# Performance work log

Measured on AMD Instinct MI355X. Metric: run time of the kernel, lower is better.

## Reference

```python
import jax, jax.numpy as jnp
import numpy as np

N, M, P, H = 200000, 20, 64, 256
EPS = 1e-12  # inside sqrt: avoids NaN grads when duplicate neighbors give zero distance


def setup_inputs() -> dict:
    key = jax.random.key(0)
    ks = jax.random.split(key, 8)
    x = jax.random.normal(ks[0], (N, P), jnp.float32)
    pos = jax.random.uniform(ks[1], (N, 2), jnp.float32) * 10.0
    y = jax.random.normal(ks[2], (N,), jnp.float32)
    # m distinct-from-self neighbor indices per node (offset trick avoids self loops)
    off = jax.random.randint(ks[3], (N, M), 1, N)
    nbr_idx = ((jnp.arange(N)[:, None] + off) % N).astype(jnp.int32)
    theta = jnp.array([1.0, 1.0, 0.1], jnp.float32)  # (sigma_sq, phi, tau)
    w1 = jax.random.normal(ks[4], (P, H), jnp.float32) * (1.0 / np.sqrt(P))
    b1 = jnp.zeros((H,), jnp.float32)
    w2 = jax.random.normal(ks[5], (H, 1), jnp.float32) * (1.0 / np.sqrt(H))
    b2 = jnp.zeros((1,), jnp.float32)
    return dict(x=x, pos=pos, y=y, nbr_idx=nbr_idx, theta=theta,
                w1=w1, b1=b1, w2=w2, b2=b2)


def _dist(a, b):
    return jnp.sqrt(jnp.sum((a - b) ** 2, axis=-1) + EPS)


def reference(x, pos, y, nbr_idx, theta, w1, b1, w2, b2):
    sigma_sq, phi, tau = theta[0], theta[1], theta[2]
    tau_sq = tau * sigma_sq
    m = nbr_idx.shape[1]
    pos_nbr = pos[nbr_idx]                                            # [N,M,2] gather
    # Cov(i, N(i)): exponential covariance of node-to-neighbor distances  [N,M]
    cov_i_ni = sigma_sq * jnp.exp(-phi * _dist(pos[:, None, :], pos_nbr))
    # Cov(N(i), N(i)) + nugget on the diagonal                          [N,M,M]
    d_nn = _dist(pos_nbr[:, :, None, :], pos_nbr[:, None, :, :])
    cov = sigma_sq * jnp.exp(-phi * d_nn) + tau_sq * jnp.eye(m, dtype=pos.dtype)
    # B_i = Cov(N,N)^{-1} Cov(i,N)  (batched small solve == inv @ vec)  [N,M]
    b_i = jnp.linalg.solve(cov, cov_i_ni[..., None])[..., 0]
    f_i = sigma_sq + tau - jnp.sum(b_i * cov_i_ni, axis=1)             # [N]
    inv_sqrt_f = 1.0 / jnp.sqrt(f_i)
    # MLP: Linear -> ReLU -> Linear, squeezed to [N]
    o = (jax.nn.relu(x @ w1 + b1) @ w2 + b2)[:, 0]
    y_decor = (y - jnp.sum(y[nbr_idx] * b_i, axis=1)) * inv_sqrt_f
    o_decor = (o - jnp.sum(o[nbr_idx] * b_i, axis=1)) * inv_sqrt_f
    return (y_decor, o_decor, o)
```

## Files before the change

kernel.cpp:

```cpp
#include <hip/hip_runtime.h>


#define MM   20
#define PP   64
#define HH   256
#define EPSF 1e-12f

#define CSE(j, r) csx[2*(j)*((j)+1) + (r)]
#define C20(r)    csx[60 + (r)]

typedef __attribute__((ext_vector_type(8))) short bf16x8;
typedef __attribute__((ext_vector_type(4))) float f32x4;

static __device__ __forceinline__ unsigned short f2bf(float f) {
    unsigned int u = __builtin_bit_cast(unsigned int, f);
    u += 0x7fffu + ((u >> 16) & 1u);
    return (unsigned short)(u >> 16);
}
static __device__ __forceinline__ float bf2f(unsigned short h) {
    unsigned int u = ((unsigned int)h) << 16;
    return __builtin_bit_cast(float, u);
}

__global__ __launch_bounds__(256, 2)
void mlp_mfma_kernel(const float* __restrict__ x,
                     const float* __restrict__ w1,
                     const float* __restrict__ b1,
                     const float* __restrict__ w2,
                     const float* __restrict__ b2,
                     float* __restrict__ o_out, int n)
{
    __shared__ __align__(16) short swh[PP * HH];
    __shared__ __align__(16) short swl[PP * HH];
    __shared__ float sb1[HH];
    __shared__ float sw2[HH];
    const int tid = threadIdx.x;

    {
        const int col = tid;
        const int t = col >> 4, nn = col & 15;
        #pragma unroll
        for (int g = 0; g < 8; ++g) {
            const int s = g >> 2, q = g & 3;
            bf16x8 hv, lv;
            #pragma unroll
            for (int u = 0; u < 8; ++u) {
                float v = w1[(g * 8 + u) * HH + col];
                unsigned short h = f2bf(v);
                hv[u] = (short)h;
                lv[u] = (short)f2bf(v - bf2f(h));
            }
            const int base = ((((t * 2 + s) * 4 + q) * 16) + nn) * 8;
            *(bf16x8*)&swh[base] = hv;
            *(bf16x8*)&swl[base] = lv;
        }
        sb1[tid] = b1[tid];
        sw2[tid] = w2[tid];
    }
    __syncthreads();

    const int lane = tid & 63;
    const int wv   = tid >> 6;
    const int nn   = lane & 15;
    const int q    = lane >> 4;
    const int wb   = blockIdx.x * 128 + wv * 32;

    bf16x8 ah[2][2], al[2][2];
    #pragma unroll
    for (int mt = 0; mt < 2; ++mt) {
        const int row = wb + mt * 16 + nn;
        #pragma unroll
        for (int s = 0; s < 2; ++s) {
            float v[8];
            if (row < n) {
                const float* xp = x + (size_t)row * PP + s * 32 + q * 8;
                float4 va = *(const float4*)(xp);
                float4 vb = *(const float4*)(xp + 4);
                v[0]=va.x; v[1]=va.y; v[2]=va.z; v[3]=va.w;
                v[4]=vb.x; v[5]=vb.y; v[6]=vb.z; v[7]=vb.w;
            } else {
                #pragma unroll
                for (int u = 0; u < 8; ++u) v[u] = 0.0f;
            }
            bf16x8 h, l;
            #pragma unroll
            for (int u = 0; u < 8; ++u) {
                unsigned short hb = f2bf(v[u]);
                h[u] = (short)hb;
                l[u] = (short)f2bf(v[u] - bf2f(hb));
            }
            ah[mt][s] = h;
            al[mt][s] = l;
        }
    }

    float part[2][4];
    #pragma unroll
    for (int mt = 0; mt < 2; ++mt)
        #pragma unroll
        for (int r = 0; r < 4; ++r) part[mt][r] = 0.0f;

    #pragma unroll
    for (int t = 0; t < 16; ++t) {
        f32x4 acc[2];
        #pragma unroll
        for (int mt = 0; mt < 2; ++mt) acc[mt] = (f32x4)(0.0f);
        #pragma unroll
        for (int s = 0; s < 2; ++s) {
            const int fb = ((((t * 2 + s) * 4 + q) * 16) + nn) * 8;
            bf16x8 bh = *(const bf16x8*)&swh[fb];
            bf16x8 bl = *(const bf16x8*)&swl[fb];
            #pragma unroll
            for (int mt = 0; mt < 2; ++mt) {
                acc[mt] = __builtin_amdgcn_mfma_f32_16x16x32_bf16(ah[mt][s], bh, acc[mt], 0, 0, 0);
                acc[mt] = __builtin_amdgcn_mfma_f32_16x16x32_bf16(al[mt][s], bh, acc[mt], 0, 0, 0);
                acc[mt] = __builtin_amdgcn_mfma_f32_16x16x32_bf16(ah[mt][s], bl, acc[mt], 0, 0, 0);
            }
        }
        const float b1t = sb1[t * 16 + nn];
        const float w2t = sw2[t * 16 + nn];
        #pragma unroll
        for (int mt = 0; mt < 2; ++mt)
            #pragma unroll
            for (int r = 0; r < 4; ++r)
                part[mt][r] = fmaf(fmaxf(acc[mt][r] + b1t, 0.0f), w2t, part[mt][r]);
    }

    #pragma unroll
    for (int w = 1; w < 16; w <<= 1)
        #pragma unroll
        for (int mt = 0; mt < 2; ++mt)
            #pragma unroll
            for (int r = 0; r < 4; ++r)
                part[mt][r] += __shfl_xor(part[mt][r], w, 64);

    const float bb = b2[0];
    if (nn == 0) {
        #pragma unroll
        for (int mt = 0; mt < 2; ++mt) {
            const int row = wb + mt * 16 + q * 4;
            if (row < n) {
                float4 o4 = make_float4(part[mt][0] + bb, part[mt][1] + bb,
                                        part[mt][2] + bb, part[mt][3] + bb);
                *(float4*)&o_out[row] = o4;
            }
        }
    }
}

#define QSWZ(v, s) __builtin_bit_cast(float, __builtin_amdgcn_ds_swizzle( \
    __builtin_bit_cast(int, (v)), 0x8000 | (0x55 * (s))))

#define GATH(R) mall[R] = QSWZ(mv[(R) >> 2], (R) & 3);

#define SCASE(K, P) case K: {                                              \
    _Pragma("unroll")                                                      \
    for (int j = (P); j < 5; ++j) pk[j] = CSE(j, (K));                     \
    p20 = C20(K); pbv = bv[K];                                             \
    pd  = QSWZ(pk[(P)], (K) & 3);                                          \
} break;

__global__ __launch_bounds__(256, 2)
void solve_kernel(const float* __restrict__ pos,
                  const float* __restrict__ y,
                  const int*   __restrict__ nbr,
                  const float* __restrict__ theta,
                  const float* __restrict__ o_in,
                  float* __restrict__ yd,
                  float* __restrict__ od, int n)
{
    const int tid  = threadIdx.x;
    const int h_   = tid & 3;
    const int i    = blockIdx.x * 64 + (tid >> 2);
    if (i >= n) return;

    const float sigma_sq = theta[0];
    const float phi      = theta[1];
    const float tau      = theta[2];
    const float tau_sq   = tau * sigma_sq;

    const float L2E = 1.44269504088896340736f;
    const float c1  = -phi * L2E;
    const float c0  = __builtin_amdgcn_logf(sigma_sq);

    const float sqrtEPS = __builtin_amdgcn_sqrtf(EPSF);
    const float diagA   = __builtin_amdgcn_exp2f(fmaf(sqrtEPS, c1, c0)) + tau_sq;
    const float diagB   = sigma_sq + tau;

    int idx[MM];
    const int4* nb4 = (const int4*)(nbr + (size_t)i * MM);
    #pragma unroll
    for (int k = 0; k < MM / 4; ++k) {
        int4 v = nb4[k];
        idx[4*k] = v.x; idx[4*k+1] = v.y; idx[4*k+2] = v.z; idx[4*k+3] = v.w;
    }

    float px[21], py[21];
    const float2* pos2 = (const float2*)pos;
    #pragma unroll
    for (int j = 0; j < MM; ++j) {
        float2 p = pos2[idx[j]];
        px[j] = p.x; py[j] = p.y;
    }
    {
        float2 p = pos2[i];
        px[20] = p.x; py[20] = p.y;
    }

    float cx[5], cy[5];
    #pragma unroll
    for (int j = 0; j < 5; ++j) {
        int cj = nbr[(size_t)i * MM + 4*j + h_];
        float2 p = pos2[cj];
        cx[j] = p.x; cy[j] = p.y;
    }

    float bv[21];
    {
        const float* src = (h_ & 1) ? o_in : y;
        #pragma unroll
        for (int j = 0; j < MM; ++j) bv[j] = src[idx[j]];
        bv[20] = src[i];
    }

    float csx[81];
    #pragma unroll
    for (int j = 0; j < 5; ++j) {
        #pragma unroll
        for (int r = 0; r <= 4*j + 3; ++r) {
            float dx = px[r] - cx[j];
            float dy = py[r] - cy[j];
            float d  = __builtin_amdgcn_sqrtf(fmaf(dx, dx, fmaf(dy, dy, EPSF)));
            float v  = __builtin_amdgcn_exp2f(fmaf(d, c1, c0));
            v = (r == 4*j + h_) ? diagA : v;
            CSE(j, r) = v;
        }
    }
    #pragma unroll
    for (int r = 0; r < 20; ++r) {
        float dx = px[r] - px[20];
        float dy = py[r] - py[20];
        float d  = __builtin_amdgcn_sqrtf(fmaf(dx, dx, fmaf(dy, dy, EPSF)));
        C20(r)   = __builtin_amdgcn_exp2f(fmaf(d, c1, c0));
    }
    C20(20) = diagB;

    float pk[5], mv[5], mall[21], p20, pbv, pd;

    #pragma unroll 1
    for (int k = 0; k < 4; ++k) {
        switch (k) {
        SCASE(0,0) SCASE(1,0) SCASE(2,0) SCASE(3,0)
        default: break;
        }
        float rp = __builtin_amdgcn_rcpf(pd);
        rp = rp * (2.0f - pd * rp);
        #pragma unroll
        for (int j = 0; j < 5; ++j)
            mv[j] = (4*j + h_ > k) ? pk[j] * rp : 0.0f;
        GATH(0)  GATH(1)  GATH(2)  GATH(3)  GATH(4)  GATH(5)  GATH(6)
        GATH(7)  GATH(8)  GATH(9)  GATH(10) GATH(11) GATH(12) GATH(13)
        GATH(14) GATH(15) GATH(16) GATH(17) GATH(18) GATH(19)
        mall[20] = p20 * rp;
        #pragma unroll
        for (int j = 0; j < 5; ++j) {
            float pkj = pk[j];
            #pragma unroll
            for (int r = 0; r <= 4*j + 3; ++r)
                CSE(j, r) = fmaf(-mall[r], pkj, CSE(j, r));
        }
        #pragma unroll
        for (int r = 0; r <= 20; ++r) {
            C20(r) = fmaf(-mall[r], p20, C20(r));
            bv[r]  = fmaf(-mall[r], pbv, bv[r]);
        }
    }

    #pragma unroll 1
    for (int k = 4; k < 8; ++k) {
        switch (k) {
        SCASE(4,1) SCASE(5,1) SCASE(6,1) SCASE(7,1)
        default: break;
        }
        float rp = __builtin_amdgcn_rcpf(pd);
        rp = rp * (2.0f - pd * rp);
        #pragma unroll
        for (int j = 1; j < 5; ++j)
            mv[j] = (4*j + h_ > k) ? pk[j] * rp : 0.0f;
        GATH(4)  GATH(5)  GATH(6)  GATH(7)  GATH(8)  GATH(9)  GATH(10)
        GATH(11) GATH(12) GATH(13) GATH(14) GATH(15) GATH(16) GATH(17)
        GATH(18) GATH(19)
        mall[20] = p20 * rp;
        #pragma unroll
        for (int j = 1; j < 5; ++j) {
            float pkj = pk[j];
            #pragma unroll
            for (int r = 4; r <= 4*j + 3; ++r)
                CSE(j, r) = fmaf(-mall[r], pkj, CSE(j, r));
        }
        #pragma unroll
        for (int r = 4; r <= 20; ++r) {
            C20(r) = fmaf(-mall[r], p20, C20(r));
            bv[r]  = fmaf(-mall[r], pbv, bv[r]);
        }
    }

    #pragma unroll 1
    for (int k = 8; k < 12; ++k) {
        switch (k) {
        SCASE(8,2) SCASE(9,2) SCASE(10,2) SCASE(11,2)
        default: break;
        }
        float rp = __builtin_amdgcn_rcpf(pd);
        rp = rp * (2.0f - pd * rp);
        #pragma unroll
        for (int j = 2; j < 5; ++j)
            mv[j] = (4*j + h_ > k) ? pk[j] * rp : 0.0f;
        GATH(8)  GATH(9)  GATH(10) GATH(11) GATH(12) GATH(13) GATH(14)
        GATH(15) GATH(16) GATH(17) GATH(18) GATH(19)
        mall[20] = p20 * rp;
        #pragma unroll
        for (int j = 2; j < 5; ++j) {
            float pkj = pk[j];
            #pragma unroll
            for (int r = 8; r <= 4*j + 3; ++r)
                CSE(j, r) = fmaf(-mall[r], pkj, CSE(j, r));
        }
        #pragma unroll
        for (int r = 8; r <= 20; ++r) {
            C20(r) = fmaf(-mall[r], p20, C20(r));
            bv[r]  = fmaf(-mall[r], pbv, bv[r]);
        }
    }

    #pragma unroll 1
    for (int k = 12; k < 16; ++k) {
        switch (k) {
        SCASE(12,3) SCASE(13,3) SCASE(14,3) SCASE(15,3)
        default: break;
        }
        float rp = __builtin_amdgcn_rcpf(pd);
        rp = rp * (2.0f - pd * rp);
        #pragma unroll
        for (int j = 3; j < 5; ++j)
            mv[j] = (4*j + h_ > k) ? pk[j] * rp : 0.0f;
        GATH(12) GATH(13) GATH(14) GATH(15) GATH(16) GATH(17) GATH(18)
        GATH(19)
        mall[20] = p20 * rp;
        #pragma unroll
        for (int j = 3; j < 5; ++j) {
            float pkj = pk[j];
            #pragma unroll
            for (int r = 12; r <= 4*j + 3; ++r)
                CSE(j, r) = fmaf(-mall[r], pkj, CSE(j, r));
        }
        #pragma unroll
        for (int r = 12; r <= 20; ++r) {
            C20(r) = fmaf(-mall[r], p20, C20(r));
            bv[r]  = fmaf(-mall[r], pbv, bv[r]);
        }
    }

    #pragma unroll 1
    for (int k = 16; k < 20; ++k) {
        switch (k) {
        SCASE(16,4) SCASE(17,4) SCASE(18,4) SCASE(19,4)
        default: break;
        }
        float rp = __builtin_amdgcn_rcpf(pd);
        rp = rp * (2.0f - pd * rp);
        mv[4] = (16 + h_ > k) ? pk[4] * rp : 0.0f;
        GATH(16) GATH(17) GATH(18) GATH(19)
        mall[20] = p20 * rp;
        {
            float pkj = pk[4];
            #pragma unroll
            for (int r = 16; r <= 19; ++r)
                CSE(4, r) = fmaf(-mall[r], pkj, CSE(4, r));
        }
        #pragma unroll
        for (int r = 16; r <= 20; ++r) {
            C20(r) = fmaf(-mall[r], p20, C20(r));
            bv[r]  = fmaf(-mall[r], pbv, bv[r]);
        }
    }

    float f  = C20(20);
    float is = __builtin_amdgcn_rsqf(f);
    is = is * fmaf(-0.5f * f * is, is, 1.5f);

    if (h_ == 0)      yd[i] = bv[20] * is;
    else if (h_ == 1) od[i] = bv[20] * is;
}

extern "C" void kernel_launch(void* const* d_in, const int* in_sizes, int n_in,
                              void* d_out, int out_size, void* d_ws, size_t ws_size,
                              hipStream_t stream)
{
    const float* x     = (const float*)d_in[0];
    const float* pos   = (const float*)d_in[1];
    const float* y     = (const float*)d_in[2];
    const int*   nbr   = (const int*)  d_in[3];
    const float* theta = (const float*)d_in[4];
    const float* w1    = (const float*)d_in[5];
    const float* b1    = (const float*)d_in[6];
    const float* w2    = (const float*)d_in[7];
    const float* b2    = (const float*)d_in[8];

    const int n = in_sizes[2];
    float* out = (float*)d_out;
    float* yd = out;
    float* od = out + (size_t)n;
    float* oo = out + 2 * (size_t)n;

    mlp_mfma_kernel<<<(n + 127) / 128, 256, 0, stream>>>(x, w1, b1, w2, b2, oo, n);
    solve_kernel<<<(n + 63) / 64, 256, 0, stream>>>(pos, y, nbr, theta, oo, yd, od, n);
}
```

Baseline: 195.8 us.

## Split the augmented column and RHS across lane pairs to raise solver occupancy

The solve kernel previously kept the full 21-entry augmented column (C20) and the RHS vector (bv) replicated in each of the 4 lanes per node. Each lane pair now holds half of these rows (11 each), and the pivot, RHS and gather values are fetched with ds_swizzle patterns. This cuts VGPR use by about 40 registers per lane, which allows raising launch bounds from 2 to 3 blocks per SIMD. In exchange it adds extra swizzles and re-reads neighbor indices and positions to build the split arrays.

```diff
diff --git a/kernel.cpp b/kernel.cpp
--- a/kernel.cpp
+++ b/kernel.cpp
@@ -7,7 +7,6 @@
 #define EPSF 1e-12f
 
 #define CSE(j, r) csx[2*(j)*((j)+1) + (r)]
-#define C20(r)    csx[60 + (r)]
 
 typedef __attribute__((ext_vector_type(8))) short bf16x8;
 typedef __attribute__((ext_vector_type(4))) float f32x4;
@@ -148,19 +147,23 @@
     }
 }
 
-#define QSWZ(v, s) __builtin_bit_cast(float, __builtin_amdgcn_ds_swizzle( \
-    __builtin_bit_cast(int, (v)), 0x8000 | (0x55 * (s))))
-
-#define GATH(R) mall[R] = QSWZ(mv[(R) >> 2], (R) & 3);
+#define QSWZ(v, pat) __builtin_bit_cast(float, __builtin_amdgcn_ds_swizzle( \
+    __builtin_bit_cast(int, (v)), 0x8000 | (pat)))
+
+#define GATH(R) mall[R] = QSWZ(mv[(R) >> 2], 0x55 * ((R) & 3));
+#define BMG(S)  bm[S]   = QSWZ(mv[(S) >> 1], ((S) & 1) ? 0xFA : 0x50);
 
 #define SCASE(K, P) case K: {                                              \
     _Pragma("unroll")                                                      \
     for (int j = (P); j < 5; ++j) pk[j] = CSE(j, (K));                     \
-    p20 = C20(K); pbv = bv[K];                                             \
-    pd  = QSWZ(pk[(P)], (K) & 3);                                          \
+    float pbs = bvl[(K) >> 1];                                             \
+    float p2s = c20l[(K) >> 1];                                            \
+    pd  = QSWZ(pk[(P)], 0x55 * ((K) & 3));                                 \
+    pbv = QSWZ(pbs, ((K) & 1) ? 0xEE : 0x44);                              \
+    p20 = QSWZ(p2s, ((K) & 1) ? 0xAA : 0x00);                              \
 } break;
 
-__global__ __launch_bounds__(256, 2)
+__global__ __launch_bounds__(256, 3)
 void solve_kernel(const float* __restrict__ pos,
                   const float* __restrict__ y,
                   const int*   __restrict__ nbr,
@@ -171,6 +174,7 @@
 {
     const int tid  = threadIdx.x;
     const int h_   = tid & 3;
+    const int q2   = h_ >> 1;
     const int i    = blockIdx.x * 64 + (tid >> 2);
     if (i >= n) return;
 
@@ -215,15 +219,24 @@
         cx[j] = p.x; cy[j] = p.y;
     }
 
-    float bv[21];
+    float bvl[11], c20l[11];
     {
         const float* src = (h_ & 1) ? o_in : y;
         #pragma unroll
-        for (int j = 0; j < MM; ++j) bv[j] = src[idx[j]];
-        bv[20] = src[i];
-    }
-
-    float csx[81];
+        for (int s = 0; s < 10; ++s) {
+            int jr = nbr[(size_t)i * MM + 2*s + q2];
+            bvl[s] = src[jr];
+            float2 p = pos2[jr];
+            float dx = p.x - px[20];
+            float dy = p.y - py[20];
+            float d  = __builtin_amdgcn_sqrtf(fmaf(dx, dx, fmaf(dy, dy, EPSF)));
+            c20l[s]  = __builtin_amdgcn_exp2f(fmaf(d, c1, c0));
+        }
+        bvl[10]  = q2 ? 0.0f : src[i];
+        c20l[10] = q2 ? 0.0f : diagB;
+    }
+
+    float csx[60];
     #pragma unroll
     for (int j = 0; j < 5; ++j) {
         #pragma unroll
@@ -236,16 +249,8 @@
             CSE(j, r) = v;
         }
     }
-    #pragma unroll
-    for (int r = 0; r < 20; ++r) {
-        float dx = px[r] - px[20];
-        float dy = py[r] - py[20];
-        float d  = __builtin_amdgcn_sqrtf(fmaf(dx, dx, fmaf(dy, dy, EPSF)));
-        C20(r)   = __builtin_amdgcn_exp2f(fmaf(d, c1, c0));
-    }
-    C20(20) = diagB;
-
-    float pk[5], mv[5], mall[21], p20, pbv, pd;
+
+    float pk[5], mv[5], mall[20], bm[11], p20, pbv, pd;
 
     #pragma unroll 1
     for (int k = 0; k < 4; ++k) {
@@ -261,7 +266,8 @@
         GATH(0)  GATH(1)  GATH(2)  GATH(3)  GATH(4)  GATH(5)  GATH(6)
         GATH(7)  GATH(8)  GATH(9)  GATH(10) GATH(11) GATH(12) GATH(13)
         GATH(14) GATH(15) GATH(16) GATH(17) GATH(18) GATH(19)
-        mall[20] = p20 * rp;
+        BMG(0) BMG(1) BMG(2) BMG(3) BMG(4) BMG(5) BMG(6) BMG(7) BMG(8) BMG(9)
+        bm[10] = p20 * rp;
         #pragma unroll
         for (int j = 0; j < 5; ++j) {
             float pkj = pk[j];
@@ -270,9 +276,9 @@
                 CSE(j, r) = fmaf(-mall[r], pkj, CSE(j, r));
         }
         #pragma unroll
-        for (int r = 0; r <= 20; ++r) {
-            C20(r) = fmaf(-mall[r], p20, C20(r));
-            bv[r]  = fmaf(-mall[r], pbv, bv[r]);
+        for (int s = 0; s <= 10; ++s) {
+            c20l[s] = fmaf(-bm[s], p20, c20l[s]);
+            bvl[s]  = fmaf(-bm[s], pbv, bvl[s]);
         }
     }
 
@@ -290,7 +296,8 @@
         GATH(4)  GATH(5)  GATH(6)  GATH(7)  GATH(8)  GATH(9)  GATH(10)
         GATH(11) GATH(12) GATH(13) GATH(14) GATH(15) GATH(16) GATH(17)
         GATH(18) GATH(19)
-        mall[20] = p20 * rp;
+        BMG(2) BMG(3) BMG(4) BMG(5) BMG(6) BMG(7) BMG(8) BMG(9)
+        bm[10] = p20 * rp;
         #pragma unroll
         for (int j = 1; j < 5; ++j) {
             float pkj = pk[j];
@@ -299,9 +306,9 @@
                 CSE(j, r) = fmaf(-mall[r], pkj, CSE(j, r));
         }
         #pragma unroll
-        for (int r = 4; r <= 20; ++r) {
-            C20(r) = fmaf(-mall[r], p20, C20(r));
-            bv[r]  = fmaf(-mall[r], pbv, bv[r]);
+        for (int s = 2; s <= 10; ++s) {
+            c20l[s] = fmaf(-bm[s], p20, c20l[s]);
+            bvl[s]  = fmaf(-bm[s], pbv, bvl[s]);
         }
     }
 
@@ -318,7 +325,8 @@
             mv[j] = (4*j + h_ > k) ? pk[j] * rp : 0.0f;
         GATH(8)  GATH(9)  GATH(10) GATH(11) GATH(12) GATH(13) GATH(14)
         GATH(15) GATH(16) GATH(17) GATH(18) GATH(19)
-        mall[20] = p20 * rp;
+        BMG(4) BMG(5) BMG(6) BMG(7) BMG(8) BMG(9)
+        bm[10] = p20 * rp;
         #pragma unroll
         for (int j = 2; j < 5; ++j) {
             float pkj = pk[j];
@@ -327,9 +335,9 @@
                 CSE(j, r) = fmaf(-mall[r], pkj, CSE(j, r));
         }
         #pragma unroll
-        for (int r = 8; r <= 20; ++r) {
-            C20(r) = fmaf(-mall[r], p20, C20(r));
-            bv[r]  = fmaf(-mall[r], pbv, bv[r]);
+        for (int s = 4; s <= 10; ++s) {
+            c20l[s] = fmaf(-bm[s], p20, c20l[s]);
+            bvl[s]  = fmaf(-bm[s], pbv, bvl[s]);
         }
     }
 
@@ -346,7 +354,8 @@
             mv[j] = (4*j + h_ > k) ? pk[j] * rp : 0.0f;
         GATH(12) GATH(13) GATH(14) GATH(15) GATH(16) GATH(17) GATH(18)
         GATH(19)
-        mall[20] = p20 * rp;
+        BMG(6) BMG(7) BMG(8) BMG(9)
+        bm[10] = p20 * rp;
         #pragma unroll
         for (int j = 3; j < 5; ++j) {
             float pkj = pk[j];
@@ -355,9 +364,9 @@
                 CSE(j, r) = fmaf(-mall[r], pkj, CSE(j, r));
         }
         #pragma unroll
-        for (int r = 12; r <= 20; ++r) {
-            C20(r) = fmaf(-mall[r], p20, C20(r));
-            bv[r]  = fmaf(-mall[r], pbv, bv[r]);
+        for (int s = 6; s <= 10; ++s) {
+            c20l[s] = fmaf(-bm[s], p20, c20l[s]);
+            bvl[s]  = fmaf(-bm[s], pbv, bvl[s]);
         }
     }
 
@@ -371,7 +380,8 @@
         rp = rp * (2.0f - pd * rp);
         mv[4] = (16 + h_ > k) ? pk[4] * rp : 0.0f;
         GATH(16) GATH(17) GATH(18) GATH(19)
-        mall[20] = p20 * rp;
+        BMG(8) BMG(9)
+        bm[10] = p20 * rp;
         {
             float pkj = pk[4];
             #pragma unroll
@@ -379,18 +389,18 @@
                 CSE(4, r) = fmaf(-mall[r], pkj, CSE(4, r));
         }
         #pragma unroll
-        for (int r = 16; r <= 20; ++r) {
-            C20(r) = fmaf(-mall[r], p20, C20(r));
-            bv[r]  = fmaf(-mall[r], pbv, bv[r]);
-        }
-    }
-
-    float f  = C20(20);
+        for (int s = 8; s <= 10; ++s) {
+            c20l[s] = fmaf(-bm[s], p20, c20l[s]);
+            bvl[s]  = fmaf(-bm[s], pbv, bvl[s]);
+        }
+    }
+
+    float f  = c20l[10];
     float is = __builtin_amdgcn_rsqf(f);
     is = is * fmaf(-0.5f * f * is, is, 1.5f);
 
-    if (h_ == 0)      yd[i] = bv[20] * is;
-    else if (h_ == 1) od[i] = bv[20] * is;
+    if (h_ == 0)      yd[i] = bvl[10] * is;
+    else if (h_ == 1) od[i] = bvl[10] * is;
 }
 
 extern "C" void kernel_launch(void* const* d_in, const int* in_sizes, int n_in,
```

Result: slower. 219.2 us (+12.0%).

## Co-schedule MLP and covariance solve in one launch; apply weights in epilogue

Applied to the files above, without the earlier changes.

Merges the MLP and solve kernels into one launch whose blocks are interleaved (one MLP block per two solve blocks), so MFMA work and VALU-heavy factorization can overlap on the GPU. The solve no longer carries y/o right-hand sides through elimination. Instead it back-substitutes for b_i, scales by 1/sqrt(f) and writes weights to workspace. A new epilogue kernel gathers y and o at the neighbors and applies those weights. This removes the dependency of the solve on the MLP output. The cost is an extra workspace write and read of about 24 floats per node, plus a serial back-substitution with shuffles.

```diff
diff --git a/kernel.cpp b/kernel.cpp
--- a/kernel.cpp
+++ b/kernel.cpp
@@ -5,6 +5,7 @@
 #define PP   64
 #define HH   256
 #define EPSF 1e-12f
+#define WSTR 24
 
 #define CSE(j, r) csx[2*(j)*((j)+1) + (r)]
 #define C20(r)    csx[60 + (r)]
@@ -22,170 +23,411 @@
     return __builtin_bit_cast(float, u);
 }
 
+#define QSWZ(v, pat) __builtin_bit_cast(float, __builtin_amdgcn_ds_swizzle( \
+    __builtin_bit_cast(int, (v)), 0x8000 | (pat)))
+
+#define GATH(R) mall[R] = QSWZ(mv[(R) >> 2], 0x55 * ((R) & 3));
+
+#define SCASE(K, P) case K: {                                              \
+    _Pragma("unroll")                                                      \
+    for (int j = (P); j < 5; ++j) pk[j] = CSE(j, (K));                     \
+    p20 = C20(K);                                                          \
+    pd  = QSWZ(pk[(P)], 0x55 * ((K) & 3));                                 \
+} break;
+
+#define BSTEP(R, JMIN) {                                                   \
+    float acc = 0.0f;                                                      \
+    _Pragma("unroll")                                                      \
+    for (int j = (JMIN); j < 5; ++j) {                                     \
+        float t = CSE(j, (R)) * bl[j];                                     \
+        acc += (4*j + h_ > (R)) ? t : 0.0f;                                \
+    }                                                                      \
+    acc += __shfl_xor(acc, 1, 64);                                         \
+    acc += __shfl_xor(acc, 2, 64);                                         \
+    float pdr = QSWZ(CSE((R) >> 2, (R)), 0x55 * ((R) & 3));                \
+    float rr = __builtin_amdgcn_rcpf(pdr);                                 \
+    rr = rr * (2.0f - pdr * rr);                                           \
+    float bR = (C20(R) - acc) * rr;                                        \
+    if (((R) & 3) == h_) bl[(R) >> 2] = bR;                                \
+}
+
 __global__ __launch_bounds__(256, 2)
-void mlp_mfma_kernel(const float* __restrict__ x,
-                     const float* __restrict__ w1,
-                     const float* __restrict__ b1,
-                     const float* __restrict__ w2,
-                     const float* __restrict__ b2,
-                     float* __restrict__ o_out, int n)
+void fused_kernel(const float* __restrict__ x,
+                  const float* __restrict__ w1,
+                  const float* __restrict__ b1,
+                  const float* __restrict__ w2,
+                  const float* __restrict__ b2,
+                  const float* __restrict__ pos,
+                  const int*   __restrict__ nbr,
+                  const float* __restrict__ theta,
+                  float* __restrict__ o_out,
+                  float* __restrict__ wis,
+                  int n, int nm)
 {
     __shared__ __align__(16) short swh[PP * HH];
     __shared__ __align__(16) short swl[PP * HH];
     __shared__ float sb1[HH];
     __shared__ float sw2[HH];
+
+    const int b   = blockIdx.x;
+    const int grp = b / 3;
+    const int rem = b - grp * 3;
     const int tid = threadIdx.x;
 
+    if (rem == 1 && grp < nm) {
+        {
+            const int col = tid;
+            const int t = col >> 4, nn = col & 15;
+            #pragma unroll
+            for (int g = 0; g < 8; ++g) {
+                const int s = g >> 2, q = g & 3;
+                bf16x8 hv, lv;
+                #pragma unroll
+                for (int u = 0; u < 8; ++u) {
+                    float v = w1[(g * 8 + u) * HH + col];
+                    unsigned short h = f2bf(v);
+                    hv[u] = (short)h;
+                    lv[u] = (short)f2bf(v - bf2f(h));
+                }
+                const int base = ((((t * 2 + s) * 4 + q) * 16) + nn) * 8;
+                *(bf16x8*)&swh[base] = hv;
+                *(bf16x8*)&swl[base] = lv;
+            }
+            sb1[tid] = b1[tid];
+            sw2[tid] = w2[tid];
+        }
+        __syncthreads();
+
+        const int lane = tid & 63;
+        const int wv   = tid >> 6;
+        const int nn   = lane & 15;
+        const int q    = lane >> 4;
+        const int wb   = grp * 128 + wv * 32;
+
+        bf16x8 ah[2][2], al[2][2];
+        #pragma unroll
+        for (int mt = 0; mt < 2; ++mt) {
+            const int row = wb + mt * 16 + nn;
+            #pragma unroll
+            for (int s = 0; s < 2; ++s) {
+                float v[8];
+                if (row < n) {
+                    const float* xp = x + (size_t)row * PP + s * 32 + q * 8;
+                    float4 va = *(const float4*)(xp);
+                    float4 vb = *(const float4*)(xp + 4);
+                    v[0]=va.x; v[1]=va.y; v[2]=va.z; v[3]=va.w;
+                    v[4]=vb.x; v[5]=vb.y; v[6]=vb.z; v[7]=vb.w;
+                } else {
+                    #pragma unroll
+                    for (int u = 0; u < 8; ++u) v[u] = 0.0f;
+                }
+                bf16x8 h, l;
+                #pragma unroll
+                for (int u = 0; u < 8; ++u) {
+                    unsigned short hb = f2bf(v[u]);
+                    h[u] = (short)hb;
+                    l[u] = (short)f2bf(v[u] - bf2f(hb));
+                }
+                ah[mt][s] = h;
+                al[mt][s] = l;
+            }
+        }
+
+        float part[2][4];
+        #pragma unroll
+        for (int mt = 0; mt < 2; ++mt)
+            #pragma unroll
+            for (int r = 0; r < 4; ++r) part[mt][r] = 0.0f;
+
+        #pragma unroll
+        for (int t = 0; t < 16; ++t) {
+            f32x4 acc[2];
+            #pragma unroll
+            for (int mt = 0; mt < 2; ++mt) acc[mt] = (f32x4)(0.0f);
+            #pragma unroll
+            for (int s = 0; s < 2; ++s) {
+                const int fb = ((((t * 2 + s) * 4 + q) * 16) + nn) * 8;
+                bf16x8 bh = *(const bf16x8*)&swh[fb];
+                bf16x8 bl2 = *(const bf16x8*)&swl[fb];
+                #pragma unroll
+                for (int mt = 0; mt < 2; ++mt) {
+                    acc[mt] = __builtin_amdgcn_mfma_f32_16x16x32_bf16(ah[mt][s], bh,  acc[mt], 0, 0, 0);
+                    acc[mt] = __builtin_amdgcn_mfma_f32_16x16x32_bf16(al[mt][s], bh,  acc[mt], 0, 0, 0);
+                    acc[mt] = __builtin_amdgcn_mfma_f32_16x16x32_bf16(ah[mt][s], bl2, acc[mt], 0, 0, 0);
+                }
+            }
+            const float b1t = sb1[t * 16 + nn];
+            const float w2t = sw2[t * 16 + nn];
+            #pragma unroll
+            for (int mt = 0; mt < 2; ++mt)
+                #pragma unroll
+                for (int r = 0; r < 4; ++r)
+                    part[mt][r] = fmaf(fmaxf(acc[mt][r] + b1t, 0.0f), w2t, part[mt][r]);
+        }
+
+        #pragma unroll
+        for (int w = 1; w < 16; w <<= 1)
+            #pragma unroll
+            for (int mt = 0; mt < 2; ++mt)
+                #pragma unroll
+                for (int r = 0; r < 4; ++r)
+                    part[mt][r] += __shfl_xor(part[mt][r], w, 64);
+
+        const float bb = b2[0];
+        if (nn == 0) {
+            #pragma unroll
+            for (int mt = 0; mt < 2; ++mt) {
+                const int row = wb + mt * 16 + q * 4;
+                if (row < n) {
+                    float4 o4 = make_float4(part[mt][0] + bb, part[mt][1] + bb,
+                                            part[mt][2] + bb, part[mt][3] + bb);
+                    *(float4*)&o_out[row] = o4;
+                }
+            }
+        }
+        return;
+    }
+
     {
-        const int col = tid;
-        const int t = col >> 4, nn = col & 15;
-        #pragma unroll
-        for (int g = 0; g < 8; ++g) {
-            const int s = g >> 2, q = g & 3;
-            bf16x8 hv, lv;
-            #pragma unroll
-            for (int u = 0; u < 8; ++u) {
-                float v = w1[(g * 8 + u) * HH + col];
-                unsigned short h = f2bf(v);
-                hv[u] = (short)h;
-                lv[u] = (short)f2bf(v - bf2f(h));
-            }
-            const int base = ((((t * 2 + s) * 4 + q) * 16) + nn) * 8;
-            *(bf16x8*)&swh[base] = hv;
-            *(bf16x8*)&swl[base] = lv;
-        }
-        sb1[tid] = b1[tid];
-        sw2[tid] = w2[tid];
+        int mcnt = (b + 1) / 3; if (mcnt > nm) mcnt = nm;
+        const int sidx = b - mcnt;
+        const int h_   = tid & 3;
+        const int i    = sidx * 64 + (tid >> 2);
+        if (i >= n) return;
+
+        const float sigma_sq = theta[0];
+        const float phi      = theta[1];
+        const float tau      = theta[2];
+        const float tau_sq   = tau * sigma_sq;
+
+        const float L2E = 1.44269504088896340736f;
+        const float c1  = -phi * L2E;
+        const float c0  = __builtin_amdgcn_logf(sigma_sq);
+
+        const float sqrtEPS = __builtin_amdgcn_sqrtf(EPSF);
+        const float diagA   = __builtin_amdgcn_exp2f(fmaf(sqrtEPS, c1, c0)) + tau_sq;
+        const float diagB   = sigma_sq + tau;
+
+        int idx[MM];
+        const int4* nb4 = (const int4*)(nbr + (size_t)i * MM);
+        #pragma unroll
+        for (int k = 0; k < MM / 4; ++k) {
+            int4 v = nb4[k];
+            idx[4*k] = v.x; idx[4*k+1] = v.y; idx[4*k+2] = v.z; idx[4*k+3] = v.w;
+        }
+
+        float px[21], py[21];
+        const float2* pos2 = (const float2*)pos;
+        #pragma unroll
+        for (int j = 0; j < MM; ++j) {
+            float2 p = pos2[idx[j]];
+            px[j] = p.x; py[j] = p.y;
+        }
+        {
+            float2 p = pos2[i];
+            px[20] = p.x; py[20] = p.y;
+        }
+
+        float cx[5], cy[5];
+        #pragma unroll
+        for (int j = 0; j < 5; ++j) {
+            int cj = nbr[(size_t)i * MM + 4*j + h_];
+            float2 p = pos2[cj];
+            cx[j] = p.x; cy[j] = p.y;
+        }
+
+        float csx[81];
+        #pragma unroll
+        for (int j = 0; j < 5; ++j) {
+            #pragma unroll
+            for (int r = 0; r <= 4*j + 3; ++r) {
+                float dx = px[r] - cx[j];
+                float dy = py[r] - cy[j];
+                float d  = __builtin_amdgcn_sqrtf(fmaf(dx, dx, fmaf(dy, dy, EPSF)));
+                float v  = __builtin_amdgcn_exp2f(fmaf(d, c1, c0));
+                v = (r == 4*j + h_) ? diagA : v;
+                CSE(j, r) = v;
+            }
+        }
+        #pragma unroll
+        for (int r = 0; r < 20; ++r) {
+            float dx = px[r] - px[20];
+            float dy = py[r] - py[20];
+            float d  = __builtin_amdgcn_sqrtf(fmaf(dx, dx, fmaf(dy, dy, EPSF)));
+            C20(r)   = __builtin_amdgcn_exp2f(fmaf(d, c1, c0));
+        }
+        C20(20) = diagB;
+
+        float pk[5], mv[5], mall[21], p20, pd;
+
+        #pragma unroll 1
+        for (int k = 0; k < 4; ++k) {
+            switch (k) {
+            SCASE(0,0) SCASE(1,0) SCASE(2,0) SCASE(3,0)
+            default: break;
+            }
+            float rp = __builtin_amdgcn_rcpf(pd);
+            rp = rp * (2.0f - pd * rp);
+            #pragma unroll
+            for (int j = 0; j < 5; ++j)
+                mv[j] = (4*j + h_ > k) ? pk[j] * rp : 0.0f;
+            GATH(0)  GATH(1)  GATH(2)  GATH(3)  GATH(4)  GATH(5)  GATH(6)
+            GATH(7)  GATH(8)  GATH(9)  GATH(10) GATH(11) GATH(12) GATH(13)
+            GATH(14) GATH(15) GATH(16) GATH(17) GATH(18) GATH(19)
+            mall[20] = p20 * rp;
+            #pragma unroll
+            for (int j = 0; j < 5; ++j) {
+                float pkj = pk[j];
+                #pragma unroll
+                for (int r = 0; r <= 4*j + 3; ++r)
+                    CSE(j, r) = fmaf(-mall[r], pkj, CSE(j, r));
+            }
+            #pragma unroll
+            for (int r = 0; r <= 20; ++r)
+                C20(r) = fmaf(-mall[r], p20, C20(r));
+        }
+
+        #pragma unroll 1
+        for (int k = 4; k < 8; ++k) {
+            switch (k) {
+            SCASE(4,1) SCASE(5,1) SCASE(6,1) SCASE(7,1)
+            default: break;
+            }
+            float rp = __builtin_amdgcn_rcpf(pd);
+            rp = rp * (2.0f - pd * rp);
+            #pragma unroll
+            for (int j = 1; j < 5; ++j)
+                mv[j] = (4*j + h_ > k) ? pk[j] * rp : 0.0f;
+            GATH(4)  GATH(5)  GATH(6)  GATH(7)  GATH(8)  GATH(9)  GATH(10)
+            GATH(11) GATH(12) GATH(13) GATH(14) GATH(15) GATH(16) GATH(17)
+            GATH(18) GATH(19)
+            mall[20] = p20 * rp;
+            #pragma unroll
+            for (int j = 1; j < 5; ++j) {
+                float pkj = pk[j];
+                #pragma unroll
+                for (int r = 4; r <= 4*j + 3; ++r)
+                    CSE(j, r) = fmaf(-mall[r], pkj, CSE(j, r));
+            }
+            #pragma unroll
+            for (int r = 4; r <= 20; ++r)
+                C20(r) = fmaf(-mall[r], p20, C20(r));
+        }
+
+        #pragma unroll 1
+        for (int k = 8; k < 12; ++k) {
+            switch (k) {
+            SCASE(8,2) SCASE(9,2) SCASE(10,2) SCASE(11,2)
+            default: break;
+            }
+            float rp = __builtin_amdgcn_rcpf(pd);
+            rp = rp * (2.0f - pd * rp);
+            #pragma unroll
+            for (int j = 2; j < 5; ++j)
+                mv[j] = (4*j + h_ > k) ? pk[j] * rp : 0.0f;
+            GATH(8)  GATH(9)  GATH(10) GATH(11) GATH(12) GATH(13) GATH(14)
+            GATH(15) GATH(16) GATH(17) GATH(18) GATH(19)
+            mall[20] = p20 * rp;
+            #pragma unroll
+            for (int j = 2; j < 5; ++j) {
+                float pkj = pk[j];
+                #pragma unroll
+                for (int r = 8; r <= 4*j + 3; ++r)
+                    CSE(j, r) = fmaf(-mall[r], pkj, CSE(j, r));
+            }
+            #pragma unroll
+            for (int r = 8; r <= 20; ++r)
+                C20(r) = fmaf(-mall[r], p20, C20(r));
+        }
+
+        #pragma unroll 1
+        for (int k = 12; k < 16; ++k) {
+            switch (k) {
+            SCASE(12,3) SCASE(13,3) SCASE(14,3) SCASE(15,3)
+            default: break;
+            }
+            float rp = __builtin_amdgcn_rcpf(pd);
+            rp = rp * (2.0f - pd * rp);
+            #pragma unroll
+            for (int j = 3; j < 5; ++j)
+                mv[j] = (4*j + h_ > k) ? pk[j] * rp : 0.0f;
+            GATH(12) GATH(13) GATH(14) GATH(15) GATH(16) GATH(17) GATH(18)
+            GATH(19)
+            mall[20] = p20 * rp;
+            #pragma unroll
+            for (int j = 3; j < 5; ++j) {
+                float pkj = pk[j];
+                #pragma unroll
+                for (int r = 12; r <= 4*j + 3; ++r)
+                    CSE(j, r) = fmaf(-mall[r], pkj, CSE(j, r));
+            }
+            #pragma unroll
+            for (int r = 12; r <= 20; ++r)
+                C20(r) = fmaf(-mall[r], p20, C20(r));
+        }
+
+        #pragma unroll 1
+        for (int k = 16; k < 20; ++k) {
+            switch (k) {
+            SCASE(16,4) SCASE(17,4) SCASE(18,4) SCASE(19,4)
+            default: break;
+            }
+            float rp = __builtin_amdgcn_rcpf(pd);
+            rp = rp * (2.0f - pd * rp);
+            mv[4] = (16 + h_ > k) ? pk[4] * rp : 0.0f;
+            GATH(16) GATH(17) GATH(18) GATH(19)
+            mall[20] = p20 * rp;
+            {
+                float pkj = pk[4];
+                #pragma unroll
+                for (int r = 16; r <= 19; ++r)
+                    CSE(4, r) = fmaf(-mall[r], pkj, CSE(4, r));
+            }
+            #pragma unroll
+            for (int r = 16; r <= 20; ++r)
+                C20(r) = fmaf(-mall[r], p20, C20(r));
+        }
+
+        float bl[5];
+        BSTEP(19,5) BSTEP(18,4) BSTEP(17,4) BSTEP(16,4)
+        BSTEP(15,4) BSTEP(14,3) BSTEP(13,3) BSTEP(12,3)
+        BSTEP(11,3) BSTEP(10,2) BSTEP(9,2)  BSTEP(8,2)
+        BSTEP(7,2)  BSTEP(6,1)  BSTEP(5,1)  BSTEP(4,1)
+        BSTEP(3,1)  BSTEP(2,0)  BSTEP(1,0)  BSTEP(0,0)
+
+        float f  = C20(20);
+        float is = __builtin_amdgcn_rsqf(f);
+        is = is * fmaf(-0.5f * f * is, is, 1.5f);
+
+        float* wp = wis + (size_t)i * WSTR;
+        #pragma unroll
+        for (int j = 0; j < 5; ++j)
+            wp[4*j + h_] = bl[j] * is;
+        if (h_ == 0) wp[20] = is;
     }
-    __syncthreads();
-
-    const int lane = tid & 63;
-    const int wv   = tid >> 6;
-    const int nn   = lane & 15;
-    const int q    = lane >> 4;
-    const int wb   = blockIdx.x * 128 + wv * 32;
-
-    bf16x8 ah[2][2], al[2][2];
-    #pragma unroll
-    for (int mt = 0; mt < 2; ++mt) {
-        const int row = wb + mt * 16 + nn;
-        #pragma unroll
-        for (int s = 0; s < 2; ++s) {
-            float v[8];
-            if (row < n) {
-                const float* xp = x + (size_t)row * PP + s * 32 + q * 8;
-                float4 va = *(const float4*)(xp);
-                float4 vb = *(const float4*)(xp + 4);
-                v[0]=va.x; v[1]=va.y; v[2]=va.z; v[3]=va.w;
-                v[4]=vb.x; v[5]=vb.y; v[6]=vb.z; v[7]=vb.w;
-            } else {
-                #pragma unroll
-                for (int u = 0; u < 8; ++u) v[u] = 0.0f;
-            }
-            bf16x8 h, l;
-            #pragma unroll
-            for (int u = 0; u < 8; ++u) {
-                unsigned short hb = f2bf(v[u]);
-                h[u] = (short)hb;
-                l[u] = (short)f2bf(v[u] - bf2f(hb));
-            }
-            ah[mt][s] = h;
-            al[mt][s] = l;
-        }
+}
+
+__global__ __launch_bounds__(256, 4)
+void epilogue_kernel(const int*   __restrict__ nbr,
+                     const float* __restrict__ y,
+                     const float* __restrict__ o_in,
+                     const float* __restrict__ wis,
+                     float* __restrict__ yd,
+                     float* __restrict__ od, int n)
+{
+    const int i = blockIdx.x * 256 + threadIdx.x;
+    if (i >= n) return;
+
+    float wv_[20];
+    {
+        const float4* w4 = (const float4*)(wis + (size_t)i * WSTR);
+        *(float4*)&wv_[0]  = w4[0];
+        *(float4*)&wv_[4]  = w4[1];
+        *(float4*)&wv_[8]  = w4[2];
+        *(float4*)&wv_[12] = w4[3];
+        *(float4*)&wv_[16] = w4[4];
     }
-
-    float part[2][4];
-    #pragma unroll
-    for (int mt = 0; mt < 2; ++mt)
-        #pragma unroll
-        for (int r = 0; r < 4; ++r) part[mt][r] = 0.0f;
-
-    #pragma unroll
-    for (int t = 0; t < 16; ++t) {
-        f32x4 acc[2];
-        #pragma unroll
-        for (int mt = 0; mt < 2; ++mt) acc[mt] = (f32x4)(0.0f);
-        #pragma unroll
-        for (int s = 0; s < 2; ++s) {
-            const int fb = ((((t * 2 + s) * 4 + q) * 16) + nn) * 8;
-            bf16x8 bh = *(const bf16x8*)&swh[fb];
-            bf16x8 bl = *(const bf16x8*)&swl[fb];
-            #pragma unroll
-            for (int mt = 0; mt < 2; ++mt) {
-                acc[mt] = __builtin_amdgcn_mfma_f32_16x16x32_bf16(ah[mt][s], bh, acc[mt], 0, 0, 0);
-                acc[mt] = __builtin_amdgcn_mfma_f32_16x16x32_bf16(al[mt][s], bh, acc[mt], 0, 0, 0);
-                acc[mt] = __builtin_amdgcn_mfma_f32_16x16x32_bf16(ah[mt][s], bl, acc[mt], 0, 0, 0);
-            }
-        }
-        const float b1t = sb1[t * 16 + nn];
-        const float w2t = sw2[t * 16 + nn];
-        #pragma unroll
-        for (int mt = 0; mt < 2; ++mt)
-            #pragma unroll
-            for (int r = 0; r < 4; ++r)
-                part[mt][r] = fmaf(fmaxf(acc[mt][r] + b1t, 0.0f), w2t, part[mt][r]);
-    }
-
-    #pragma unroll
-    for (int w = 1; w < 16; w <<= 1)
-        #pragma unroll
-        for (int mt = 0; mt < 2; ++mt)
-            #pragma unroll
-            for (int r = 0; r < 4; ++r)
-                part[mt][r] += __shfl_xor(part[mt][r], w, 64);
-
-    const float bb = b2[0];
-    if (nn == 0) {
-        #pragma unroll
-        for (int mt = 0; mt < 2; ++mt) {
-            const int row = wb + mt * 16 + q * 4;
-            if (row < n) {
-                float4 o4 = make_float4(part[mt][0] + bb, part[mt][1] + bb,
-                                        part[mt][2] + bb, part[mt][3] + bb);
-                *(float4*)&o_out[row] = o4;
-            }
-        }
-    }
-}
-
-#define QSWZ(v, s) __builtin_bit_cast(float, __builtin_amdgcn_ds_swizzle( \
-    __builtin_bit_cast(int, (v)), 0x8000 | (0x55 * (s))))
-
-#define GATH(R) mall[R] = QSWZ(mv[(R) >> 2], (R) & 3);
-
-#define SCASE(K, P) case K: {                                              \
-    _Pragma("unroll")                                                      \
-    for (int j = (P); j < 5; ++j) pk[j] = CSE(j, (K));                     \
-    p20 = C20(K); pbv = bv[K];                                             \
-    pd  = QSWZ(pk[(P)], (K) & 3);                                          \
-} break;
-
-__global__ __launch_bounds__(256, 2)
-void solve_kernel(const float* __restrict__ pos,
-                  const float* __restrict__ y,
-                  const int*   __restrict__ nbr,
-                  const float* __restrict__ theta,
-                  const float* __restrict__ o_in,
-                  float* __restrict__ yd,
-                  float* __restrict__ od, int n)
-{
-    const int tid  = threadIdx.x;
-    const int h_   = tid & 3;
-    const int i    = blockIdx.x * 64 + (tid >> 2);
-    if (i >= n) return;
-
-    const float sigma_sq = theta[0];
-    const float phi      = theta[1];
-    const float tau      = theta[2];
-    const float tau_sq   = tau * sigma_sq;
-
-    const float L2E = 1.44269504088896340736f;
-    const float c1  = -phi * L2E;
-    const float c0  = __builtin_amdgcn_logf(sigma_sq);
-
-    const float sqrtEPS = __builtin_amdgcn_sqrtf(EPSF);
-    const float diagA   = __builtin_amdgcn_exp2f(fmaf(sqrtEPS, c1, c0)) + tau_sq;
-    const float diagB   = sigma_sq + tau;
+    const float is = wis[(size_t)i * WSTR + 20];
 
     int idx[MM];
     const int4* nb4 = (const int4*)(nbr + (size_t)i * MM);
@@ -195,202 +437,14 @@
         idx[4*k] = v.x; idx[4*k+1] = v.y; idx[4*k+2] = v.z; idx[4*k+3] = v.w;
     }
 
-    float px[21], py[21];
-    const float2* pos2 = (const float2*)pos;
+    float sy = 0.0f, so = 0.0f;
     #pragma unroll
     for (int j = 0; j < MM; ++j) {
-        float2 p = pos2[idx[j]];
-        px[j] = p.x; py[j] = p.y;
+        sy = fmaf(wv_[j], y[idx[j]],    sy);
+        so = fmaf(wv_[j], o_in[idx[j]], so);
     }
-    {
-        float2 p = pos2[i];
-        px[20] = p.x; py[20] = p.y;
-    }
-
-    float cx[5], cy[5];
-    #pragma unroll
-    for (int j = 0; j < 5; ++j) {
-        int cj = nbr[(size_t)i * MM + 4*j + h_];
-        float2 p = pos2[cj];
-        cx[j] = p.x; cy[j] = p.y;
-    }
-
-    float bv[21];
-    {
-        const float* src = (h_ & 1) ? o_in : y;
-        #pragma unroll
-        for (int j = 0; j < MM; ++j) bv[j] = src[idx[j]];
-        bv[20] = src[i];
-    }
-
-    float csx[81];
-    #pragma unroll
-    for (int j = 0; j < 5; ++j) {
-        #pragma unroll
-        for (int r = 0; r <= 4*j + 3; ++r) {
-            float dx = px[r] - cx[j];
-            float dy = py[r] - cy[j];
-            float d  = __builtin_amdgcn_sqrtf(fmaf(dx, dx, fmaf(dy, dy, EPSF)));
-            float v  = __builtin_amdgcn_exp2f(fmaf(d, c1, c0));
-            v = (r == 4*j + h_) ? diagA : v;
-            CSE(j, r) = v;
-        }
-    }
-    #pragma unroll
-    for (int r = 0; r < 20; ++r) {
-        float dx = px[r] - px[20];
-        float dy = py[r] - py[20];
-        float d  = __builtin_amdgcn_sqrtf(fmaf(dx, dx, fmaf(dy, dy, EPSF)));
-        C20(r)   = __builtin_amdgcn_exp2f(fmaf(d, c1, c0));
-    }
-    C20(20) = diagB;
-
-    float pk[5], mv[5], mall[21], p20, pbv, pd;
-
-    #pragma unroll 1
-    for (int k = 0; k < 4; ++k) {
-        switch (k) {
-        SCASE(0,0) SCASE(1,0) SCASE(2,0) SCASE(3,0)
-        default: break;
-        }
-        float rp = __builtin_amdgcn_rcpf(pd);
-        rp = rp * (2.0f - pd * rp);
-        #pragma unroll
-        for (int j = 0; j < 5; ++j)
-            mv[j] = (4*j + h_ > k) ? pk[j] * rp : 0.0f;
-        GATH(0)  GATH(1)  GATH(2)  GATH(3)  GATH(4)  GATH(5)  GATH(6)
-        GATH(7)  GATH(8)  GATH(9)  GATH(10) GATH(11) GATH(12) GATH(13)
-        GATH(14) GATH(15) GATH(16) GATH(17) GATH(18) GATH(19)
-        mall[20] = p20 * rp;
-        #pragma unroll
-        for (int j = 0; j < 5; ++j) {
-            float pkj = pk[j];
-            #pragma unroll
-            for (int r = 0; r <= 4*j + 3; ++r)
-                CSE(j, r) = fmaf(-mall[r], pkj, CSE(j, r));
-        }
-        #pragma unroll
-        for (int r = 0; r <= 20; ++r) {
-            C20(r) = fmaf(-mall[r], p20, C20(r));
-            bv[r]  = fmaf(-mall[r], pbv, bv[r]);
-        }
-    }
-
-    #pragma unroll 1
-    for (int k = 4; k < 8; ++k) {
-        switch (k) {
-        SCASE(4,1) SCASE(5,1) SCASE(6,1) SCASE(7,1)
-        default: break;
-        }
-        float rp = __builtin_amdgcn_rcpf(pd);
-        rp = rp * (2.0f - pd * rp);
-        #pragma unroll
-        for (int j = 1; j < 5; ++j)
-            mv[j] = (4*j + h_ > k) ? pk[j] * rp : 0.0f;
-        GATH(4)  GATH(5)  GATH(6)  GATH(7)  GATH(8)  GATH(9)  GATH(10)
-        GATH(11) GATH(12) GATH(13) GATH(14) GATH(15) GATH(16) GATH(17)
-        GATH(18) GATH(19)
-        mall[20] = p20 * rp;
-        #pragma unroll
-        for (int j = 1; j < 5; ++j) {
-            float pkj = pk[j];
-            #pragma unroll
-            for (int r = 4; r <= 4*j + 3; ++r)
-                CSE(j, r) = fmaf(-mall[r], pkj, CSE(j, r));
-        }
-        #pragma unroll
-        for (int r = 4; r <= 20; ++r) {
-            C20(r) = fmaf(-mall[r], p20, C20(r));
-            bv[r]  = fmaf(-mall[r], pbv, bv[r]);
-        }
-    }
-
-    #pragma unroll 1
-    for (int k = 8; k < 12; ++k) {
-        switch (k) {
-        SCASE(8,2) SCASE(9,2) SCASE(10,2) SCASE(11,2)
-        default: break;
-        }
-        float rp = __builtin_amdgcn_rcpf(pd);
-        rp = rp * (2.0f - pd * rp);
-        #pragma unroll
-        for (int j = 2; j < 5; ++j)
-            mv[j] = (4*j + h_ > k) ? pk[j] * rp : 0.0f;
-        GATH(8)  GATH(9)  GATH(10) GATH(11) GATH(12) GATH(13) GATH(14)
-        GATH(15) GATH(16) GATH(17) GATH(18) GATH(19)
-        mall[20] = p20 * rp;
-        #pragma unroll
-        for (int j = 2; j < 5; ++j) {
-            float pkj = pk[j];
-            #pragma unroll
-            for (int r = 8; r <= 4*j + 3; ++r)
-                CSE(j, r) = fmaf(-mall[r], pkj, CSE(j, r));
-        }
-        #pragma unroll
-        for (int r = 8; r <= 20; ++r) {
-            C20(r) = fmaf(-mall[r], p20, C20(r));
-            bv[r]  = fmaf(-mall[r], pbv, bv[r]);
-        }
-    }
-
-    #pragma unroll 1
-    for (int k = 12; k < 16; ++k) {
-        switch (k) {
-        SCASE(12,3) SCASE(13,3) SCASE(14,3) SCASE(15,3)
-        default: break;
-        }
-        float rp = __builtin_amdgcn_rcpf(pd);
-        rp = rp * (2.0f - pd * rp);
-        #pragma unroll
-        for (int j = 3; j < 5; ++j)
-            mv[j] = (4*j + h_ > k) ? pk[j] * rp : 0.0f;
-        GATH(12) GATH(13) GATH(14) GATH(15) GATH(16) GATH(17) GATH(18)
-        GATH(19)
-        mall[20] = p20 * rp;
-        #pragma unroll
-        for (int j = 3; j < 5; ++j) {
-            float pkj = pk[j];
-            #pragma unroll
-            for (int r = 12; r <= 4*j + 3; ++r)
-                CSE(j, r) = fmaf(-mall[r], pkj, CSE(j, r));
-        }
-        #pragma unroll
-        for (int r = 12; r <= 20; ++r) {
-            C20(r) = fmaf(-mall[r], p20, C20(r));
-            bv[r]  = fmaf(-mall[r], pbv, bv[r]);
-        }
-    }
-
-    #pragma unroll 1
-    for (int k = 16; k < 20; ++k) {
-        switch (k) {
-        SCASE(16,4) SCASE(17,4) SCASE(18,4) SCASE(19,4)
-        default: break;
-        }
-        float rp = __builtin_amdgcn_rcpf(pd);
-        rp = rp * (2.0f - pd * rp);
-        mv[4] = (16 + h_ > k) ? pk[4] * rp : 0.0f;
-        GATH(16) GATH(17) GATH(18) GATH(19)
-        mall[20] = p20 * rp;
-        {
-            float pkj = pk[4];
-            #pragma unroll
-            for (int r = 16; r <= 19; ++r)
-                CSE(4, r) = fmaf(-mall[r], pkj, CSE(4, r));
-        }
-        #pragma unroll
-        for (int r = 16; r <= 20; ++r) {
-            C20(r) = fmaf(-mall[r], p20, C20(r));
-            bv[r]  = fmaf(-mall[r], pbv, bv[r]);
-        }
-    }
-
-    float f  = C20(20);
-    float is = __builtin_amdgcn_rsqf(f);
-    is = is * fmaf(-0.5f * f * is, is, 1.5f);
-
-    if (h_ == 0)      yd[i] = bv[20] * is;
-    else if (h_ == 1) od[i] = bv[20] * is;
+    yd[i] = fmaf(is, y[i],    -sy);
+    od[i] = fmaf(is, o_in[i], -so);
 }
 
 extern "C" void kernel_launch(void* const* d_in, const int* in_sizes, int n_in,
@@ -412,7 +466,12 @@
     float* yd = out;
     float* od = out + (size_t)n;
     float* oo = out + 2 * (size_t)n;
-
-    mlp_mfma_kernel<<<(n + 127) / 128, 256, 0, stream>>>(x, w1, b1, w2, b2, oo, n);
-    solve_kernel<<<(n + 63) / 64, 256, 0, stream>>>(pos, y, nbr, theta, oo, yd, od, n);
-}
+    float* wis = (float*)d_ws;
+
+    const int nm = (n + 127) / 128;
+    const int ns = (n + 63) / 64;
+    fused_kernel<<<nm + ns, 256, 0, stream>>>(x, w1, b1, w2, b2,
+                                              pos, nbr, theta, oo, wis, n, nm);
+    epilogue_kernel<<<(n + 255) / 256, 256, 0, stream>>>(nbr, y, oo, wis,
+                                                         yd, od, n);
+}
```

After: 228.7 us. +16.8%, slower.
